# Optimization experiments

Hardware: AMD Instinct MI355X
Metric: run time of the kernel (lower is better)

Reference implementation:

```python
import jax, jax.numpy as jnp
import numpy as np
from jax import lax

MB, NS, Z_DIM, R_DIM, HID, NUM_STEPS = 128, 64, 64, 128, 512, 100
B = MB * NS
T_TOTAL = 1.0
ETA = 1.0
DT = T_TOTAL / NUM_STEPS
LOG2PI = float(np.log(2.0 * np.pi))


def setup_inputs() -> dict:
    key = jax.random.key(0)
    ks = jax.random.split(key, 8)
    in_dim = Z_DIM + R_DIM + 1
    return {
        "r": jax.random.normal(ks[0], (MB, NS, R_DIM), jnp.float32),
        "noises": jax.random.normal(ks[1], (B, NUM_STEPS, Z_DIM), jnp.float32),
        "x0": jax.random.normal(ks[2], (B, Z_DIM), jnp.float32) * ETA,  # prior sample, std=eta
        "W1": jax.random.normal(ks[3], (in_dim, HID), jnp.float32) / np.sqrt(in_dim),
        "b1": jnp.zeros((HID,), jnp.float32),
        "W2": jax.random.normal(ks[4], (HID, Z_DIM), jnp.float32) / np.sqrt(HID),
        "b2": jnp.zeros((Z_DIM,), jnp.float32),
        "beta_max": jnp.float32(10.0),
        "beta_min": jnp.float32(0.01),
        "target_mu": jax.random.normal(ks[5], (Z_DIM,), jnp.float32),
    }


def reference(r, noises, x0, W1, b1, W2, b2, beta_max, beta_min, target_mu):
    # cosine-squared schedule (analytic integrals), per update_schedules()
    C_start = jax.nn.softplus(beta_max)
    C_end = jax.nn.softplus(beta_min)
    a = C_start - C_end
    b = jnp.pi / (2.0 * T_TOTAL)
    c = C_end

    def F(t):  # forward integrated scheduler \int_0^t
        return a * jnp.sin(2.0 * b * t) / (4.0 * b) + a * t / 2.0 + c * t

    steps = jnp.arange(NUM_STEPS + 1, dtype=jnp.float32)
    alpha = 1.0 - jnp.exp(-2.0 * (F((steps + 1.0) * DT) - F(steps * DT)))  # [S+1]
    kappa = (ETA * (1.0 - jnp.sqrt(1.0 - alpha))) ** 2 / alpha              # [S+1]

    r_flat = r.reshape(B, R_DIM)

    def control(t, x):  # score network: MLP on concat(x, r, t)
        t_feat = jnp.full((B, 1), t, dtype=x.dtype)
        h = jnp.tanh(jnp.concatenate([x, r_flat, t_feat], axis=-1) @ W1 + b1)
        return h @ W2 + b2

    def step(carry, xs):
        x, lw = carry
        t, al, ka, noise = xs
        score = control(t, x)
        means = x + (1.0 - jnp.sqrt(1.0 - al)) * (2.0 * ETA ** 2 * score - x)
        std = ETA * jnp.sqrt(al)
        x_new = means + std * noise
        lw_det = -2.0 * ka * jnp.sum(score ** 2, axis=-1)
        lw_sto = -2.0 * jnp.sqrt(ka) * jnp.sum(score * noise, axis=-1)
        return (x_new, lw + lw_det + lw_sto), x_new

    xs = (
        jnp.arange(NUM_STEPS, dtype=jnp.float32) * DT,
        alpha[:NUM_STEPS],
        kappa[:NUM_STEPS],
        jnp.swapaxes(noises, 0, 1),  # [S, B, D]
    )
    (x, lw), x_hist = lax.scan(step, (x0, jnp.zeros((B,), x0.dtype)), xs)

    x_t = jnp.swapaxes(jnp.concatenate([x0[None], x_hist], axis=0), 0, 1)  # [B, S+1, D]

    # terminal weight: log target - log prior (both diagonal Normals)
    target_lp = jnp.sum(-0.5 * (x - target_mu) ** 2 - 0.5 * LOG2PI, axis=-1)
    prior_lp = jnp.sum(-0.5 * (x / ETA) ** 2 - 0.5 * LOG2PI - jnp.log(jnp.float32(ETA)), axis=-1)
    log_weights = lw + target_lp - prior_lp

    # nabla_g = prior_score(x) - target_score(x)
    nabla_g = (-x / ETA ** 2) - (-(x - target_mu))
    return x_t, log_weights, nabla_g
```

## Files before the change

kernel.cpp:

```cpp
#include <hip/hip_runtime.h>

#define ZD 64
#define RD 128
#define HIDDEN 512
#define NSTEP 100
#define OUT_PITCH 6464
#define DT_F 0.01f
#define ROWS 32

static const size_t LW_OFF = 52953088ull;
static const size_t NG_OFF = 52961280ull;

typedef __attribute__((ext_vector_type(2))) float  f32x2;
typedef __attribute__((ext_vector_type(4))) float  f32x4;
typedef __attribute__((ext_vector_type(8))) __bf16 bf16x8;
typedef __attribute__((ext_vector_type(2))) short  s16x2;
typedef __attribute__((ext_vector_type(4))) short  s16x4;
typedef __attribute__((ext_vector_type(8))) short  s16x8;

__device__ __forceinline__ short f2bs(float f) {
    return __builtin_bit_cast(short, (__bf16)f);
}
__device__ __forceinline__ float tanh_fast(float x) {
    float e = __builtin_amdgcn_exp2f(x * 2.88539008177793f);
    float r = __builtin_amdgcn_rcpf(e + 1.0f);
    return fmaf(-2.0f, r, 1.0f);
}

__global__ __launch_bounds__(1024, 1)
void sim_kernel(
    const float* __restrict__ r, const float* __restrict__ noises,
    const float* __restrict__ x0, const float* __restrict__ W1,
    const float* __restrict__ b1, const float* __restrict__ W2,
    const float* __restrict__ b2, const float* __restrict__ bmax,
    const float* __restrict__ bmin, const float* __restrict__ mu,
    float* __restrict__ out)
{
    __shared__ float Ps[4][ROWS][72];
    __shared__ unsigned short Xb[ROWS * 64];
    __shared__ unsigned short Hs[ROWS * HIDDEN];
    __shared__ float w1ts[HIDDEN];
    __shared__ float tT[NSTEP], tG[NSTEP], tSd[NSTEP], tCd[NSTEP], tCs[NSTEP];

    const int tid  = threadIdx.x;
    const int lane = tid & 63;
    const int wave = tid >> 6;
    const int g4   = lane >> 4;
    const int l16  = lane & 15;
    const int row0 = blockIdx.x * ROWS;

    if (tid < NSTEP) {
        float spmax = log1pf(expf(bmax[0]));
        float spmin = log1pf(expf(bmin[0]));
        float a_ = spmax - spmin;
        float c_ = spmin;
        const float PI_ = 3.14159265358979323846f;
        float k = (float)tid;
        float t0 = k * DT_F, t1 = (k + 1.0f) * DT_F;
        float inv2pi = 1.0f / (2.0f * PI_);
        float F0 = a_ * sinf(PI_ * t0) * inv2pi + (0.5f * a_ + c_) * t0;
        float F1 = a_ * sinf(PI_ * t1) * inv2pi + (0.5f * a_ + c_) * t1;
        float al = 1.0f - expf(-2.0f * (F1 - F0));
        float gg = 1.0f - sqrtf(1.0f - al);
        float kap = (gg * gg) / al;
        tT[tid] = t0; tG[tid] = gg; tSd[tid] = sqrtf(al);
        tCd[tid] = -2.0f * kap; tCs[tid] = -2.0f * sqrtf(kap);
    }
    if (tid < HIDDEN) w1ts[tid] = W1[(size_t)192 * HIDDEN + tid];

    const int urow = tid >> 5;
    const int c2   = (tid & 31) * 2;
    const size_t ubase = (size_t)(row0 + urow);
    float xr0, xr1;
    {
        f32x2 v = *(const f32x2*)(x0 + ubase * ZD + c2);
        xr0 = v[0]; xr1 = v[1];
        *(f32x2*)(out + ubase * OUT_PITCH + c2) = v;
        s16x2 xv; xv[0] = f2bs(xr0); xv[1] = f2bs(xr1);
        *(s16x2*)(Xb + ((urow * 64 + c2) ^ ((urow & 7) << 3))) = xv;
    }
    const float bb0 = b2[c2], bb1 = b2[c2 + 1];

    f32x4 pref[2][2];
    {
        #pragma unroll
        for (int mtt = 0; mtt < 2; ++mtt) {
            bf16x8 rf[4];
            const float* rp = r + (size_t)(row0 + mtt * 16 + l16) * RD;
            #pragma unroll
            for (int kc = 0; kc < 4; ++kc) {
                f32x4 lo = *(const f32x4*)(rp + kc * 32 + g4 * 8);
                f32x4 hi = *(const f32x4*)(rp + kc * 32 + g4 * 8 + 4);
                bf16x8 v;
                v[0]=(__bf16)lo[0]; v[1]=(__bf16)lo[1]; v[2]=(__bf16)lo[2]; v[3]=(__bf16)lo[3];
                v[4]=(__bf16)hi[0]; v[5]=(__bf16)hi[1]; v[6]=(__bf16)hi[2]; v[7]=(__bf16)hi[3];
                rf[kc] = v;
            }
            #pragma unroll
            for (int j2 = 0; j2 < 2; ++j2) {
                int n  = (wave * 2 + j2) * 16 + l16;
                int n0 = (wave * 2 + j2) * 16 + g4 * 4;
                f32x4 acc = *(const f32x4*)(b1 + n0);
                #pragma unroll
                for (int kc = 0; kc < 4; ++kc) {
                    bf16x8 w;
                    #pragma unroll
                    for (int j = 0; j < 8; ++j)
                        w[j] = (__bf16)W1[(size_t)(64 + kc * 32 + g4 * 8 + j) * HIDDEN + n];
                    acc = __builtin_amdgcn_mfma_f32_16x16x32_bf16(w, rf[kc], acc, 0, 0, 0);
                }
                pref[j2][mtt] = acc;
            }
        }
    }

    bf16x8 w1f[2][2];
    #pragma unroll
    for (int j2 = 0; j2 < 2; ++j2) {
        int n = (wave * 2 + j2) * 16 + l16;
        #pragma unroll
        for (int kc = 0; kc < 2; ++kc) {
            bf16x8 v;
            #pragma unroll
            for (int j = 0; j < 8; ++j) {
                int kk = kc * 32 + g4 * 8 + j;
                v[j] = (__bf16)W1[(size_t)kk * HIDDEN + n];
            }
            w1f[j2][kc] = v;
        }
    }
    const int zh = wave & 1, kq = (wave >> 1) & 3, mtw = wave >> 3;
    bf16x8 w2f[2][4];
    #pragma unroll
    for (int zt2 = 0; zt2 < 2; ++zt2) {
        int n = (zh * 2 + zt2) * 16 + l16;
        #pragma unroll
        for (int i = 0; i < 4; ++i) {
            bf16x8 v;
            #pragma unroll
            for (int j = 0; j < 8; ++j)
                v[j] = (__bf16)W2[(size_t)(kq * 128 + i * 32 + g4 * 8 + j) * ZD + n];
            w2f[zt2][i] = v;
        }
    }

    float lwacc = 0.0f;

    __syncthreads();

    for (int s = 0; s < NSTEP; ++s) {
        float t = tT[s];
        f32x2 nz = *(const f32x2*)(noises + (ubase * NSTEP + s) * ZD + c2);

        {
            s16x8 xb[2][2];
            #pragma unroll
            for (int mtt = 0; mtt < 2; ++mtt) {
                int m = mtt * 16 + l16;
                int swz = (m & 7) << 3;
                xb[mtt][0] = *(const s16x8*)(Xb + ((m * 64 + g4 * 8) ^ swz));
                xb[mtt][1] = *(const s16x8*)(Xb + ((m * 64 + 32 + g4 * 8) ^ swz));
            }
            #pragma unroll
            for (int j2 = 0; j2 < 2; ++j2) {
                int n0 = (wave * 2 + j2) * 16 + g4 * 4;
                f32x4 wt = *(const f32x4*)(w1ts + n0);
                #pragma unroll
                for (int mtt = 0; mtt < 2; ++mtt) {
                    f32x4 acc = pref[j2][mtt];
                    acc[0] = fmaf(t, wt[0], acc[0]);
                    acc[1] = fmaf(t, wt[1], acc[1]);
                    acc[2] = fmaf(t, wt[2], acc[2]);
                    acc[3] = fmaf(t, wt[3], acc[3]);
                    acc = __builtin_amdgcn_mfma_f32_16x16x32_bf16(
                        w1f[j2][0], __builtin_bit_cast(bf16x8, xb[mtt][0]), acc, 0, 0, 0);
                    acc = __builtin_amdgcn_mfma_f32_16x16x32_bf16(
                        w1f[j2][1], __builtin_bit_cast(bf16x8, xb[mtt][1]), acc, 0, 0, 0);
                    s16x4 hv;
                    hv[0] = f2bs(tanh_fast(acc[0]));
                    hv[1] = f2bs(tanh_fast(acc[1]));
                    hv[2] = f2bs(tanh_fast(acc[2]));
                    hv[3] = f2bs(tanh_fast(acc[3]));
                    int m = mtt * 16 + l16;
                    *(s16x4*)(Hs + ((m * HIDDEN + n0) ^ ((m & 7) << 3))) = hv;
                }
            }
        }
        __syncthreads();

        {
            int m = mtw * 16 + l16;
            int swz = (m & 7) << 3;
            int base = m * HIDDEN + kq * 128 + g4 * 8;
            f32x4 aA = { 0.f, 0.f, 0.f, 0.f };
            f32x4 aB = { 0.f, 0.f, 0.f, 0.f };
            #pragma unroll
            for (int i = 0; i < 4; ++i) {
                s16x8 h = *(const s16x8*)(Hs + ((base + i * 32) ^ swz));
                aA = __builtin_amdgcn_mfma_f32_16x16x32_bf16(
                    w2f[0][i], __builtin_bit_cast(bf16x8, h), aA, 0, 0, 0);
                aB = __builtin_amdgcn_mfma_f32_16x16x32_bf16(
                    w2f[1][i], __builtin_bit_cast(bf16x8, h), aB, 0, 0, 0);
            }
            *(f32x4*)(&Ps[kq][m][(zh * 2 + 0) * 16 + g4 * 4]) = aA;
            *(f32x4*)(&Ps[kq][m][(zh * 2 + 1) * 16 + g4 * 4]) = aB;
        }
        __syncthreads();

        {
            float gg = tG[s], sdv = tSd[s], cd = tCd[s], cs = tCs[s];
            f32x2 p0 = *(const f32x2*)(&Ps[0][urow][c2]);
            f32x2 p1 = *(const f32x2*)(&Ps[1][urow][c2]);
            f32x2 p2 = *(const f32x2*)(&Ps[2][urow][c2]);
            f32x2 p3 = *(const f32x2*)(&Ps[3][urow][c2]);
            float s0 = ((p0[0] + p1[0]) + (p2[0] + p3[0])) + bb0;
            float s1 = ((p0[1] + p1[1]) + (p2[1] + p3[1])) + bb1;
            float xn0 = xr0 + gg * (2.0f * s0 - xr0) + sdv * nz[0];
            float xn1 = xr1 + gg * (2.0f * s1 - xr1) + sdv * nz[1];
            xr0 = xn0; xr1 = xn1;
            f32x2 xv = { xn0, xn1 };
            *(f32x2*)(out + ubase * OUT_PITCH + (size_t)(s + 1) * ZD + c2) = xv;
            s16x2 xb2; xb2[0] = f2bs(xn0); xb2[1] = f2bs(xn1);
            *(s16x2*)(Xb + ((urow * 64 + c2) ^ ((urow & 7) << 3))) = xb2;
            lwacc += cd * (s0 * s0 + s1 * s1) + cs * (s0 * nz[0] + s1 * nz[1]);
        }
        __syncthreads();
    }

    {
        float m0 = mu[c2], m1 = mu[c2 + 1];
        float d0 = xr0 - m0, d1 = xr1 - m1;
        f32x2 ng = { d0 - xr0, d1 - xr1 };
        *(f32x2*)(out + NG_OFF + ubase * ZD + c2) = ng;
        float part = lwacc
                   + 0.5f * (xr0 * xr0 + xr1 * xr1) - 0.5f * (d0 * d0 + d1 * d1);
        part += __shfl_xor(part, 1, 64);
        part += __shfl_xor(part, 2, 64);
        part += __shfl_xor(part, 4, 64);
        part += __shfl_xor(part, 8, 64);
        part += __shfl_xor(part, 16, 64);
        if ((tid & 31) == 0) out[LW_OFF + ubase] = part;
    }
}

extern "C" void kernel_launch(void* const* d_in, const int* in_sizes, int n_in,
                              void* d_out, int out_size, void* d_ws, size_t ws_size,
                              hipStream_t stream) {
    const float* r      = (const float*)d_in[0];
    const float* noises = (const float*)d_in[1];
    const float* x0     = (const float*)d_in[2];
    const float* W1     = (const float*)d_in[3];
    const float* b1     = (const float*)d_in[4];
    const float* W2     = (const float*)d_in[5];
    const float* b2     = (const float*)d_in[6];
    const float* bmax   = (const float*)d_in[7];
    const float* bmin   = (const float*)d_in[8];
    const float* mu     = (const float*)d_in[9];
    float* out = (float*)d_out;

    sim_kernel<<<256, 1024, 0, stream>>>(r, noises, x0, W1, b1, W2, b2,
                                         bmax, bmin, mu, out);
}
```

Measured before the change: 241.2 us.

## Halve rows per block to 16, launch 512 blocks of 512 threads

Each block now handles 16 rows with 8 waves instead of 32 rows with 16 waves, and the grid doubles to 512 blocks with launch bounds allowing two blocks per CU. Each wave covers four hidden tiles instead of two, and the precomputed r-projection is kept in registers as packed bf16 to save register space. The goal is to use more CUs on a 256-CU part and overlap the barrier-bound step loop across co-resident blocks. Storing the projection in bf16 adds rounding error, and each block's per-step critical path grows.

```diff
diff --git a/kernel.cpp b/kernel.cpp
--- a/kernel.cpp
+++ b/kernel.cpp
@@ -6,7 +6,7 @@
 #define NSTEP 100
 #define OUT_PITCH 6464
 #define DT_F 0.01f
-#define ROWS 32
+#define ROWS 16
 
 static const size_t LW_OFF = 52953088ull;
 static const size_t NG_OFF = 52961280ull;
@@ -21,13 +21,16 @@
 __device__ __forceinline__ short f2bs(float f) {
     return __builtin_bit_cast(short, (__bf16)f);
 }
+__device__ __forceinline__ float bs2f(short s) {
+    return __builtin_bit_cast(float, ((unsigned)(unsigned short)s) << 16);
+}
 __device__ __forceinline__ float tanh_fast(float x) {
     float e = __builtin_amdgcn_exp2f(x * 2.88539008177793f);
     float r = __builtin_amdgcn_rcpf(e + 1.0f);
     return fmaf(-2.0f, r, 1.0f);
 }
 
-__global__ __launch_bounds__(1024, 1)
+__global__ __launch_bounds__(512, 2)
 void sim_kernel(
     const float* __restrict__ r, const float* __restrict__ noises,
     const float* __restrict__ x0, const float* __restrict__ W1,
@@ -66,7 +69,7 @@
         tT[tid] = t0; tG[tid] = gg; tSd[tid] = sqrtf(al);
         tCd[tid] = -2.0f * kap; tCs[tid] = -2.0f * sqrtf(kap);
     }
-    if (tid < HIDDEN) w1ts[tid] = W1[(size_t)192 * HIDDEN + tid];
+    w1ts[tid] = W1[(size_t)192 * HIDDEN + tid];
 
     const int urow = tid >> 5;
     const int c2   = (tid & 31) * 2;
@@ -81,55 +84,53 @@
     }
     const float bb0 = b2[c2], bb1 = b2[c2 + 1];
 
-    f32x4 pref[2][2];
+    s16x4 prefb[4];
     {
-        #pragma unroll
-        for (int mtt = 0; mtt < 2; ++mtt) {
-            bf16x8 rf[4];
-            const float* rp = r + (size_t)(row0 + mtt * 16 + l16) * RD;
+        bf16x8 rf[4];
+        const float* rp = r + (size_t)(row0 + l16) * RD;
+        #pragma unroll
+        for (int kc = 0; kc < 4; ++kc) {
+            f32x4 lo = *(const f32x4*)(rp + kc * 32 + g4 * 8);
+            f32x4 hi = *(const f32x4*)(rp + kc * 32 + g4 * 8 + 4);
+            bf16x8 v;
+            v[0]=(__bf16)lo[0]; v[1]=(__bf16)lo[1]; v[2]=(__bf16)lo[2]; v[3]=(__bf16)lo[3];
+            v[4]=(__bf16)hi[0]; v[5]=(__bf16)hi[1]; v[6]=(__bf16)hi[2]; v[7]=(__bf16)hi[3];
+            rf[kc] = v;
+        }
+        #pragma unroll
+        for (int j2 = 0; j2 < 4; ++j2) {
+            int n  = (wave * 4 + j2) * 16 + l16;
+            int n0 = (wave * 4 + j2) * 16 + g4 * 4;
+            f32x4 acc = *(const f32x4*)(b1 + n0);
             #pragma unroll
             for (int kc = 0; kc < 4; ++kc) {
-                f32x4 lo = *(const f32x4*)(rp + kc * 32 + g4 * 8);
-                f32x4 hi = *(const f32x4*)(rp + kc * 32 + g4 * 8 + 4);
-                bf16x8 v;
-                v[0]=(__bf16)lo[0]; v[1]=(__bf16)lo[1]; v[2]=(__bf16)lo[2]; v[3]=(__bf16)lo[3];
-                v[4]=(__bf16)hi[0]; v[5]=(__bf16)hi[1]; v[6]=(__bf16)hi[2]; v[7]=(__bf16)hi[3];
-                rf[kc] = v;
+                bf16x8 w;
+                #pragma unroll
+                for (int j = 0; j < 8; ++j)
+                    w[j] = (__bf16)W1[(size_t)(64 + kc * 32 + g4 * 8 + j) * HIDDEN + n];
+                acc = __builtin_amdgcn_mfma_f32_16x16x32_bf16(w, rf[kc], acc, 0, 0, 0);
             }
-            #pragma unroll
-            for (int j2 = 0; j2 < 2; ++j2) {
-                int n  = (wave * 2 + j2) * 16 + l16;
-                int n0 = (wave * 2 + j2) * 16 + g4 * 4;
-                f32x4 acc = *(const f32x4*)(b1 + n0);
-                #pragma unroll
-                for (int kc = 0; kc < 4; ++kc) {
-                    bf16x8 w;
-                    #pragma unroll
-                    for (int j = 0; j < 8; ++j)
-                        w[j] = (__bf16)W1[(size_t)(64 + kc * 32 + g4 * 8 + j) * HIDDEN + n];
-                    acc = __builtin_amdgcn_mfma_f32_16x16x32_bf16(w, rf[kc], acc, 0, 0, 0);
-                }
-                pref[j2][mtt] = acc;
-            }
-        }
-    }
-
-    bf16x8 w1f[2][2];
+            s16x4 pb;
+            pb[0] = f2bs(acc[0]); pb[1] = f2bs(acc[1]);
+            pb[2] = f2bs(acc[2]); pb[3] = f2bs(acc[3]);
+            prefb[j2] = pb;
+        }
+    }
+
+    bf16x8 w1f[4][2];
     #pragma unroll
-    for (int j2 = 0; j2 < 2; ++j2) {
-        int n = (wave * 2 + j2) * 16 + l16;
+    for (int j2 = 0; j2 < 4; ++j2) {
+        int n = (wave * 4 + j2) * 16 + l16;
         #pragma unroll
         for (int kc = 0; kc < 2; ++kc) {
             bf16x8 v;
             #pragma unroll
-            for (int j = 0; j < 8; ++j) {
-                int kk = kc * 32 + g4 * 8 + j;
-                v[j] = (__bf16)W1[(size_t)kk * HIDDEN + n];
-            }
+            for (int j = 0; j < 8; ++j)
+                v[j] = (__bf16)W1[(size_t)(kc * 32 + g4 * 8 + j) * HIDDEN + n];
             w1f[j2][kc] = v;
         }
     }
-    const int zh = wave & 1, kq = (wave >> 1) & 3, mtw = wave >> 3;
+    const int zh = wave & 1, kq = wave >> 1;
     bf16x8 w2f[2][4];
     #pragma unroll
     for (int zt2 = 0; zt2 < 2; ++zt2) {
@@ -145,6 +146,7 @@
     }
 
     float lwacc = 0.0f;
+    const int xswz = (l16 & 7) << 3;
 
     __syncthreads();
 
@@ -153,57 +155,46 @@
         f32x2 nz = *(const f32x2*)(noises + (ubase * NSTEP + s) * ZD + c2);
 
         {
-            s16x8 xb[2][2];
-            #pragma unroll
-            for (int mtt = 0; mtt < 2; ++mtt) {
-                int m = mtt * 16 + l16;
-                int swz = (m & 7) << 3;
-                xb[mtt][0] = *(const s16x8*)(Xb + ((m * 64 + g4 * 8) ^ swz));
-                xb[mtt][1] = *(const s16x8*)(Xb + ((m * 64 + 32 + g4 * 8) ^ swz));
+            s16x8 xb0 = *(const s16x8*)(Xb + ((l16 * 64 + g4 * 8) ^ xswz));
+            s16x8 xb1 = *(const s16x8*)(Xb + ((l16 * 64 + 32 + g4 * 8) ^ xswz));
+            #pragma unroll
+            for (int j2 = 0; j2 < 4; ++j2) {
+                int n0 = (wave * 4 + j2) * 16 + g4 * 4;
+                f32x4 wt = *(const f32x4*)(w1ts + n0);
+                s16x4 pb = prefb[j2];
+                f32x4 acc;
+                acc[0] = fmaf(t, wt[0], bs2f(pb[0]));
+                acc[1] = fmaf(t, wt[1], bs2f(pb[1]));
+                acc[2] = fmaf(t, wt[2], bs2f(pb[2]));
+                acc[3] = fmaf(t, wt[3], bs2f(pb[3]));
+                acc = __builtin_amdgcn_mfma_f32_16x16x32_bf16(
+                    w1f[j2][0], __builtin_bit_cast(bf16x8, xb0), acc, 0, 0, 0);
+                acc = __builtin_amdgcn_mfma_f32_16x16x32_bf16(
+                    w1f[j2][1], __builtin_bit_cast(bf16x8, xb1), acc, 0, 0, 0);
+                s16x4 hv;
+                hv[0] = f2bs(tanh_fast(acc[0]));
+                hv[1] = f2bs(tanh_fast(acc[1]));
+                hv[2] = f2bs(tanh_fast(acc[2]));
+                hv[3] = f2bs(tanh_fast(acc[3]));
+                *(s16x4*)(Hs + ((l16 * HIDDEN + n0) ^ xswz)) = hv;
             }
-            #pragma unroll
-            for (int j2 = 0; j2 < 2; ++j2) {
-                int n0 = (wave * 2 + j2) * 16 + g4 * 4;
-                f32x4 wt = *(const f32x4*)(w1ts + n0);
-                #pragma unroll
-                for (int mtt = 0; mtt < 2; ++mtt) {
-                    f32x4 acc = pref[j2][mtt];
-                    acc[0] = fmaf(t, wt[0], acc[0]);
-                    acc[1] = fmaf(t, wt[1], acc[1]);
-                    acc[2] = fmaf(t, wt[2], acc[2]);
-                    acc[3] = fmaf(t, wt[3], acc[3]);
-                    acc = __builtin_amdgcn_mfma_f32_16x16x32_bf16(
-                        w1f[j2][0], __builtin_bit_cast(bf16x8, xb[mtt][0]), acc, 0, 0, 0);
-                    acc = __builtin_amdgcn_mfma_f32_16x16x32_bf16(
-                        w1f[j2][1], __builtin_bit_cast(bf16x8, xb[mtt][1]), acc, 0, 0, 0);
-                    s16x4 hv;
-                    hv[0] = f2bs(tanh_fast(acc[0]));
-                    hv[1] = f2bs(tanh_fast(acc[1]));
-                    hv[2] = f2bs(tanh_fast(acc[2]));
-                    hv[3] = f2bs(tanh_fast(acc[3]));
-                    int m = mtt * 16 + l16;
-                    *(s16x4*)(Hs + ((m * HIDDEN + n0) ^ ((m & 7) << 3))) = hv;
-                }
-            }
         }
         __syncthreads();
 
         {
-            int m = mtw * 16 + l16;
-            int swz = (m & 7) << 3;
-            int base = m * HIDDEN + kq * 128 + g4 * 8;
+            int base = l16 * HIDDEN + kq * 128 + g4 * 8;
             f32x4 aA = { 0.f, 0.f, 0.f, 0.f };
             f32x4 aB = { 0.f, 0.f, 0.f, 0.f };
             #pragma unroll
             for (int i = 0; i < 4; ++i) {
-                s16x8 h = *(const s16x8*)(Hs + ((base + i * 32) ^ swz));
+                s16x8 h = *(const s16x8*)(Hs + ((base + i * 32) ^ xswz));
                 aA = __builtin_amdgcn_mfma_f32_16x16x32_bf16(
                     w2f[0][i], __builtin_bit_cast(bf16x8, h), aA, 0, 0, 0);
                 aB = __builtin_amdgcn_mfma_f32_16x16x32_bf16(
                     w2f[1][i], __builtin_bit_cast(bf16x8, h), aB, 0, 0, 0);
             }
-            *(f32x4*)(&Ps[kq][m][(zh * 2 + 0) * 16 + g4 * 4]) = aA;
-            *(f32x4*)(&Ps[kq][m][(zh * 2 + 1) * 16 + g4 * 4]) = aB;
+            *(f32x4*)(&Ps[kq][l16][(zh * 2 + 0) * 16 + g4 * 4]) = aA;
+            *(f32x4*)(&Ps[kq][l16][(zh * 2 + 1) * 16 + g4 * 4]) = aB;
         }
         __syncthreads();
 
@@ -258,6 +249,6 @@
     const float* mu     = (const float*)d_in[9];
     float* out = (float*)d_out;
 
-    sim_kernel<<<256, 1024, 0, stream>>>(r, noises, x0, W1, b1, W2, b2,
-                                         bmax, bmin, mu, out);
-}
+    sim_kernel<<<512, 512, 0, stream>>>(r, noises, x0, W1, b1, W2, b2,
+                                        bmax, bmin, mu, out);
+}
```

New measurement: 284.2 us. +17.8%, slower.
